# Optimization experiments

Hardware: AMD Instinct MI355X
Metric: run time of the kernel (lower is better)

The kernel has to match this reference:

```python
import jax, jax.numpy as jnp
import numpy as np

TOP_K = 8
RECENCY_DECAY = 0.99
CURRENT_TS = 1.0


def _normalize(x, eps=1e-12):
    # matches torch F.normalize: x / max(||x||_2, eps)
    n = jnp.linalg.norm(x, axis=-1, keepdims=True)
    return x / jnp.maximum(n, eps)


def setup_inputs() -> dict:
    key = jax.random.key(0)
    ks = jax.random.split(key, 7)
    B, N, H = 2048, 65536, 1024
    return {
        "query": jax.random.normal(ks[0], (B, H), dtype=jnp.float32),
        "store": jax.random.normal(ks[1], (N, H), dtype=jnp.float32),
        "importance": jax.random.uniform(ks[2], (N,), dtype=jnp.float32),
        "timestamps": jax.random.uniform(ks[3], (N,), dtype=jnp.float32),
        "Wk": jax.random.normal(ks[4], (H, H), dtype=jnp.float32) / np.sqrt(H),
        "Wv": jax.random.normal(ks[5], (H, H), dtype=jnp.float32) / np.sqrt(H),
        "Wo": jax.random.normal(ks[6], (H, H), dtype=jnp.float32) / np.sqrt(H),
    }


def reference(query, store, importance, timestamps, Wk, Wv, Wo):
    # key/value projections over the full store (Linear, no bias)
    keys = store @ Wk.T          # [N, H]
    vals = store @ Wv.T          # [N, H]

    # recency/importance weighting
    ages = CURRENT_TS - timestamps
    recency = jnp.exp(-jnp.abs(ages) * (1.0 - RECENCY_DECAY))
    weights = recency * (importance + 1.0)
    weights = weights / (weights.sum() + 1e-8)  # [N]

    # cosine similarity scaled by weights
    q_norm = _normalize(query)   # [B, H]
    k_norm = _normalize(keys)    # [N, H]
    sim = (q_norm @ k_norm.T) * weights[None, :]  # [B, N]

    # top-k retrieval + softmax-weighted combine
    topk_sim, topk_idx = jax.lax.top_k(sim, TOP_K)   # [B, k]
    attn = jax.nn.softmax(topk_sim, axis=-1)          # [B, k]
    topk_vals = vals[topk_idx]                        # [B, k, H]
    out = jnp.einsum("bk,bkh->bh", attn, topk_vals)  # [B, H]
    return out @ Wo.T
```

## Files before the change

kernel.cpp:

```cpp
#include <hip/hip_runtime.h>
#include <stdint.h>

typedef _Float16 f16;
typedef _Float16 f16x8 __attribute__((ext_vector_type(8)));
typedef _Float16 f16x4 __attribute__((ext_vector_type(4)));
typedef float    f32x4 __attribute__((ext_vector_type(4)));

#define B_DIM 2048
#define N_DIM 65536
#define H_DIM 1024

typedef const __attribute__((address_space(1))) void g_void;
typedef __attribute__((address_space(3))) void l_void;
__device__ __forceinline__ void glds16(const void* g, void* l) {
    __builtin_amdgcn_global_load_lds((g_void*)g, (l_void*)l, 16, 0, 0);
}

__global__ __launch_bounds__(256) void k_weights(const float* __restrict__ imp,
                                                 const float* __restrict__ ts,
                                                 float* __restrict__ w,
                                                 float* __restrict__ sumw) {
    int i = blockIdx.x * 256 + threadIdx.x;
    float age = 1.0f - ts[i];
    float r = expf(-fabsf(age) * (float)(1.0 - 0.99));
    float wv = r * (imp[i] + 1.0f);
    w[i] = wv;
    for (int off = 32; off; off >>= 1) wv += __shfl_down(wv, off, 64);
    __shared__ float ps[4];
    if ((threadIdx.x & 63) == 0) ps[threadIdx.x >> 6] = wv;
    __syncthreads();
    if (threadIdx.x == 0) atomicAdd(sumw, ps[0] + ps[1] + ps[2] + ps[3]);
}

__global__ __launch_bounds__(256) void k_split(const float* __restrict__ x,
                                               f16* __restrict__ hi, f16* __restrict__ lo) {
    size_t i = (size_t)blockIdx.x * 256 + threadIdx.x;
    float4 v0 = ((const float4*)x)[2 * i];
    float4 v1 = ((const float4*)x)[2 * i + 1];
    float vv[8] = {v0.x, v0.y, v0.z, v0.w, v1.x, v1.y, v1.z, v1.w};
    f16x8 h, l;
#pragma unroll
    for (int j = 0; j < 8; j++) { h[j] = (f16)vv[j]; l[j] = (f16)(vv[j] - (float)h[j]); }
    ((f16x8*)hi)[i] = h;
    ((f16x8*)lo)[i] = l;
}

__global__ __launch_bounds__(256) void k_tohalf(const float* __restrict__ x, f16* __restrict__ h) {
    size_t i = (size_t)blockIdx.x * 256 + threadIdx.x;
    float4 v0 = ((const float4*)x)[2 * i];
    float4 v1 = ((const float4*)x)[2 * i + 1];
    f16x8 o = {(f16)v0.x, (f16)v0.y, (f16)v0.z, (f16)v0.w,
               (f16)v1.x, (f16)v1.y, (f16)v1.z, (f16)v1.w};
    ((f16x8*)h)[i] = o;
}

__global__ __launch_bounds__(256) void k_tsplit(const float* __restrict__ Wm,
                                                f16* __restrict__ th, f16* __restrict__ tl_) {
    __shared__ float tl[64][65];
    const int t = threadIdx.x;
    const int r0 = blockIdx.y * 64, c0 = blockIdx.x * 64;
#pragma unroll
    for (int p = 0; p < 16; ++p) {
        int idx = p * 256 + t;
        int r = idx >> 6, c = idx & 63;
        tl[r][c] = Wm[(size_t)(r0 + r) * H_DIM + c0 + c];
    }
    __syncthreads();
#pragma unroll
    for (int p = 0; p < 16; ++p) {
        int idx = p * 256 + t;
        int oc = idx >> 6, rr = idx & 63;
        float v = tl[rr][oc];
        f16 h = (f16)v;
        th[(size_t)(c0 + oc) * H_DIM + r0 + rr] = h;
        tl_[(size_t)(c0 + oc) * H_DIM + r0 + rr] = (f16)(v - (float)h);
    }
}

__global__ __launch_bounds__(256) void k_qnorm(const float* __restrict__ q,
                                               f16* __restrict__ qh, f16* __restrict__ ql) {
    int b = blockIdx.x, t = threadIdx.x;
    float4 v = ((const float4*)(q + (size_t)b * H_DIM))[t];
    float ss = v.x * v.x + v.y * v.y + v.z * v.z + v.w * v.w;
    for (int off = 32; off; off >>= 1) ss += __shfl_down(ss, off, 64);
    __shared__ float ps[4];
    if ((t & 63) == 0) ps[t >> 6] = ss;
    __syncthreads();
    float tot = ps[0] + ps[1] + ps[2] + ps[3];
    float rn = 1.0f / fmaxf(sqrtf(tot), 1e-12f);
    float o[4] = {v.x * rn, v.y * rn, v.z * rn, v.w * rn};
    f16x4 h, l;
#pragma unroll
    for (int j = 0; j < 4; j++) { h[j] = (f16)o[j]; l[j] = (f16)(o[j] - (float)h[j]); }
    ((f16x4*)(qh + (size_t)b * H_DIM))[t] = h;
    ((f16x4*)(ql + (size_t)b * H_DIM))[t] = l;
}

__global__ __launch_bounds__(256) void k_fin(const float* __restrict__ w,
                                             const float* __restrict__ sumw,
                                             const float* __restrict__ nrm2,
                                             float* __restrict__ sscale) {
    int i = blockIdx.x * 256 + threadIdx.x;
    sscale[i] = w[i] / ((sumw[0] + 1e-8f) * fmaxf(sqrtf(nrm2[i]), 1e-12f));
}


#define RD_A(AB, H)                                                              \
    _Pragma("unroll") for (int mi = 0; mi < 4; ++mi) {                           \
        a[mi][0] = *(const f16x8*)(lds + (AB) + arow + (H)*8192 + mi*2048 + acol0); \
        a[mi][1] = *(const f16x8*)(lds + (AB) + arow + (H)*8192 + mi*2048 + acol1); \
    }

#define RD_B(DST, BB, OFFH)                                                      \
    _Pragma("unroll") for (int nj = 0; nj < 2; ++nj) {                           \
        DST[nj][0] = *(const f16x8*)(lds + (BB) + (OFFH) + brow + nj*2048 + acol0); \
        DST[nj][1] = *(const f16x8*)(lds + (BB) + (OFFH) + brow + nj*2048 + acol1); \
    }

#define PH_PRE()                                                                 \
    __builtin_amdgcn_s_barrier();                                                \
    asm volatile("s_waitcnt lgkmcnt(0)" ::: "memory");                           \
    __builtin_amdgcn_sched_barrier(0);                                           \
    __builtin_amdgcn_s_setprio(1);

#define PH_POST()                                                                \
    __builtin_amdgcn_s_setprio(0);                                               \
    __builtin_amdgcn_s_barrier();

#define MFMA8x2(MH, BV, NB)                                                      \
    _Pragma("unroll") for (int ks = 0; ks < 2; ++ks)                             \
    _Pragma("unroll") for (int mi = 0; mi < 4; ++mi)                             \
    _Pragma("unroll") for (int nj = 0; nj < 2; ++nj)                             \
        acc[(MH)*4 + mi][(NB) + nj] = __builtin_amdgcn_mfma_f32_16x16x32_f16(    \
            a[mi][ks], BV[nj][ks], acc[(MH)*4 + mi][(NB) + nj], 0, 0, 0);

#define TILE_BODY(T, STG, W0STR)                                                 \
  {                                                                              \
    const int cur = (T) & 1;                                                     \
    const int ab = cur * 32768;                                                  \
    const int bb = 65536 + cur * 32768;                                          \
    const int da = (cur ^ 1) * 32768;                                            \
    const int db = 65536 + (cur ^ 1) * 32768;                                    \
    const f16* An = A0; const f16* Bn = Bh; int toffn = 0;                       \
    if (STG) {                                                                   \
        const int tn = (T) + 1;                                                  \
        if constexpr (OUTMODE == 0) {                                            \
            An = (tn < 16) ? A0 : (tn < 32 ? A1 : A0);                           \
            Bn = (tn < 32) ? Bh : Bl;                                            \
            toffn = (tn & 15) * 64;                                              \
        } else { toffn = tn * 64; }                                              \
    }                                                                            \
                                                    \
    RD_A(ab, 0)                                                                  \
    RD_B(b0, bb, 0)                                                              \
    if (STG) {                                                                   \
        glds16(An + aoff0 + toffn, lds + da + tid * 16);                         \
        glds16(An + aoff2 + toffn, lds + da + 16384 + tid * 16);                 \
        glds16(Bn + boffE1 + toffn, lds + db + tid * 16);                        \
        glds16(Bn + boffE2 + toffn, lds + db + 8192 + tid * 16);                 \
    }                                                                            \
    asm volatile("s_waitcnt vmcnt(" W0STR ")" ::: "memory");                     \
    PH_PRE() MFMA8x2(0, b0, 0) PH_POST()                                         \
                                                     \
    RD_B(b1, bb, 16384)                                                          \
    if (STG) {                                                                   \
        glds16(Bn + boffO1 + toffn, lds + db + 16384 + tid * 16);                \
        glds16(Bn + boffO2 + toffn, lds + db + 24576 + tid * 16);                \
        glds16(An + aoff1 + toffn, lds + da + 8192 + tid * 16);                  \
        glds16(An + aoff3 + toffn, lds + da + 24576 + tid * 16);                 \
    }                                                                            \
    PH_PRE() MFMA8x2(0, b1, 2) PH_POST()                                         \
                                                     \
    RD_A(ab, 1)                                                                  \
    PH_PRE() MFMA8x2(1, b1, 2) PH_POST()                                         \
                                                    \
    asm volatile("s_waitcnt vmcnt(4)" ::: "memory");                             \
    PH_PRE() MFMA8x2(1, b0, 0) PH_POST()                                         \
  }

template <int OUTMODE>
__global__ __launch_bounds__(512) void k_gemm8(
    const f16* __restrict__ A0, const f16* __restrict__ A1,
    const f16* __restrict__ Bh, const f16* __restrict__ Bl,
    unsigned int* __restrict__ cand, const float* __restrict__ colscale,
    float* __restrict__ nrm2) {
    __shared__ char lds[131072];
    const int tid = threadIdx.x;

    constexpr int NT = (OUTMODE == 0) ? 48 : 16;

    int m0, n0;
    {
        const int f = blockIdx.x;
        if constexpr (OUTMODE == 0) {
            const int lg = (f & 7) * 128 + (f >> 3);
            m0 = (lg >> 2) * 256; n0 = (lg & 3) * 256;
        } else {
            const int lg = (f & 7) * 256 + (f >> 3);
            m0 = (lg & 7) * 256; n0 = (lg >> 3) * 256;
        }
    }

    const int sr = tid >> 3, ss = tid & 7;
    const int ssw = (ss ^ (sr & 7)) * 8;
    const size_t aoff0 = (size_t)(m0 + sr) * H_DIM + ssw;
    const size_t aoff1 = (size_t)(m0 + 64 + sr) * H_DIM + ssw;
    const size_t aoff2 = (size_t)(m0 + 128 + sr) * H_DIM + ssw;
    const size_t aoff3 = (size_t)(m0 + 192 + sr) * H_DIM + ssw;
    const int nE = (sr >> 5) * 64 + (sr & 31);
    const size_t boffE1 = (size_t)(n0 + nE) * H_DIM + ssw;
    const size_t boffE2 = (size_t)(n0 + nE + 128) * H_DIM + ssw;
    const size_t boffO1 = (size_t)(n0 + nE + 32) * H_DIM + ssw;
    const size_t boffO2 = (size_t)(n0 + nE + 160) * H_DIM + ssw;

    const int lane = tid & 63, wave = tid >> 6;
    const int wr = wave >> 2, wc = wave & 3;
    const int m16 = lane & 15, q4 = lane >> 4;
    const int axor = (lane & 7) << 4;
    const int acol0 = (q4 * 16) ^ axor;
    const int acol1 = (64 + q4 * 16) ^ axor;
    const int arow = (wr * 128 + m16) * 128;
    const int brow = (wc * 32 + m16) * 128;

    f32x4 acc[8][4];
#pragma unroll
    for (int i = 0; i < 8; i++)
#pragma unroll
        for (int j = 0; j < 4; j++) acc[i][j] = (f32x4){0.f, 0.f, 0.f, 0.f};
    f16x8 a[4][2], b0[2][2], b1[2][2];

    glds16(A0 + aoff0, lds + tid * 16);
    glds16(A0 + aoff2, lds + 16384 + tid * 16);
    glds16(Bh + boffE1, lds + 65536 + tid * 16);
    glds16(Bh + boffE2, lds + 65536 + 8192 + tid * 16);
    glds16(Bh + boffO1, lds + 65536 + 16384 + tid * 16);
    glds16(Bh + boffO2, lds + 65536 + 24576 + tid * 16);
    glds16(A0 + aoff1, lds + 8192 + tid * 16);
    glds16(A0 + aoff3, lds + 24576 + tid * 16);
    asm volatile("s_waitcnt vmcnt(4)" ::: "memory");
    __builtin_amdgcn_s_barrier();

    for (int t = 0; t < NT - 1; ++t) TILE_BODY(t, 1, "4")
    TILE_BODY(NT - 1, 0, "0")

    if constexpr (OUTMODE == 0) {
#pragma unroll
        for (int mi = 0; mi < 8; ++mi)
#pragma unroll
            for (int rr = 0; rr < 4; ++rr) {
                float s = 0.f;
#pragma unroll
                for (int njj = 0; njj < 4; ++njj) {
                    float v = acc[mi][njj][rr];
                    s += v * v;
                }
                s += __shfl_xor(s, 1, 64);
                s += __shfl_xor(s, 2, 64);
                s += __shfl_xor(s, 4, 64);
                s += __shfl_xor(s, 8, 64);
                if (m16 == 0)
                    atomicAdd(&nrm2[m0 + wr * 128 + mi * 16 + q4 * 4 + rr], s);
            }
    } else {
        float cs0 = colscale[n0 + wc * 64 + m16];
        float cs1 = colscale[n0 + wc * 64 + 16 + m16];
        float cs2 = colscale[n0 + wc * 64 + 32 + m16];
        float cs3 = colscale[n0 + wc * 64 + 48 + m16];
#pragma unroll
        for (int mi = 0; mi < 8; ++mi)
#pragma unroll
            for (int njj = 0; njj < 4; ++njj) {
                const float c = (njj == 0) ? cs0 : (njj == 1) ? cs1 : (njj == 2) ? cs2 : cs3;
#pragma unroll
                for (int rr = 0; rr < 4; ++rr) acc[mi][njj][rr] *= c;
            }

        float* ldsf = (float*)lds;
        const int r = tid >> 2;
        const int seg = tid & 3;
        const int g5 = tid & 31;
        const int chunkbase = (n0 >> 8) * 8;

#pragma unroll 1
        for (int half = 0; half < 2; ++half) {
            __syncthreads();
            if (wr == half) {
#pragma unroll
                for (int mi = 0; mi < 8; ++mi)
#pragma unroll
                    for (int njj = 0; njj < 4; ++njj)
#pragma unroll
                        for (int rr = 0; rr < 4; ++rr) {
                            int row = mi * 16 + q4 * 4 + rr;
                            int col = wc * 64 + (njj >> 1) * 32 + (njj & 1) * 16 + m16;
                            ldsf[row * 256 + col] = acc[mi][njj][rr];
                        }
            }
            __syncthreads();

            unsigned int tk[8];
#pragma unroll
            for (int i = 0; i < 8; ++i) tk[i] = 0u;
            unsigned int mn = 0u; int mslot = 0;
            for (int jj = 0; jj < 64; ++jj) {
                const int pos = seg * 64 + (jj ^ g5);
                float v = ldsf[r * 256 + pos];
                unsigned int u = __builtin_bit_cast(unsigned int, v);
                u = (u & 0x80000000u) ? ~u : (u | 0x80000000u);
                unsigned int key = (u & 0xFFFFFF00u) | (unsigned)pos;
                if (key > mn) {
#pragma unroll
                    for (int i = 0; i < 8; ++i) tk[i] = (i == mslot) ? key : tk[i];
                    mn = tk[0]; mslot = 0;
#pragma unroll
                    for (int i = 1; i < 8; ++i) { if (tk[i] < mn) { mn = tk[i]; mslot = i; } }
                }
            }
            unsigned int win0, win1, win2, win3, win4, win5, win6, win7;
#pragma unroll
            for (int e = 0; e < 8; ++e) {
                unsigned int lm = tk[0];
#pragma unroll
                for (int i = 1; i < 8; ++i) lm = max(lm, tk[i]);
                unsigned int o1 = max(lm, __shfl_xor(lm, 1, 64));
                unsigned int o2 = max(o1, __shfl_xor(o1, 2, 64));
                if (e == 0) win0 = o2; else if (e == 1) win1 = o2; else if (e == 2) win2 = o2;
                else if (e == 3) win3 = o2; else if (e == 4) win4 = o2; else if (e == 5) win5 = o2;
                else if (e == 6) win6 = o2; else win7 = o2;
#pragma unroll
                for (int i = 0; i < 8; ++i) tk[i] = (tk[i] == o2) ? 0u : tk[i];
            }
            if (seg == 0) {
                const int b = m0 + half * 128 + r;
                uint4* dst = (uint4*)(cand + (size_t)b * 2048 + chunkbase);
                dst[0] = (uint4){win0, win1, win2, win3};
                dst[1] = (uint4){win4, win5, win6, win7};
            }
        }
    }
    (void)A1; (void)Bl; (void)nrm2; (void)colscale; (void)cand;
}

template <int OUTMODE>
__global__ __launch_bounds__(256) void k_gemm64(const f16* __restrict__ A, const f16* __restrict__ Al,
                                                const f16* __restrict__ B, const f16* __restrict__ Bl,
                                                float* __restrict__ of32, f16* __restrict__ of16) {
    __shared__ f16 As[64 * 32];
    __shared__ f16 Bs[128 * 32];
    __shared__ f16 AsL[(OUTMODE == 4) ? 64 * 32 : 1];
    __shared__ f16 BsL[(OUTMODE == 4) ? 128 * 32 : 1];
    const int tid = threadIdx.x;
    const int m0 = blockIdx.y * 64, n0 = blockIdx.x * 128;
    const int r = tid >> 2, c8 = (tid & 3) * 8;
    const f16* ga = A + (size_t)(m0 + r) * H_DIM + c8;
    const f16* gb0 = B + (size_t)(n0 + r) * H_DIM + c8;
    const f16* gb1 = B + (size_t)(n0 + r + 64) * H_DIM + c8;
    const f16 *gal = nullptr, *gbl0 = nullptr, *gbl1 = nullptr;
    if constexpr (OUTMODE == 4) {
        gal = Al + (size_t)(m0 + r) * H_DIM + c8;
        gbl0 = Bl + (size_t)(n0 + r) * H_DIM + c8;
        gbl1 = Bl + (size_t)(n0 + r + 64) * H_DIM + c8;
    }

    const int lane = tid & 63, wave = tid >> 6;
    const int wn = wave * 32;
    const int q4 = lane >> 4, m16 = lane & 15;
    const int aoff = m16 * 32 + q4 * 8;
    const int boff = (wn + m16) * 32 + q4 * 8;

    f32x4 acc[4][2];
#pragma unroll
    for (int i = 0; i < 4; i++)
#pragma unroll
        for (int j = 0; j < 2; j++) acc[i][j] = (f32x4){0.f, 0.f, 0.f, 0.f};

    for (int k0 = 0; k0 < H_DIM; k0 += 32) {
        __syncthreads();
        glds16(ga + k0, As + tid * 8);
        glds16(gb0 + k0, Bs + tid * 8);
        glds16(gb1 + k0, Bs + 2048 + tid * 8);
        if constexpr (OUTMODE == 4) {
            glds16(gal + k0, AsL + tid * 8);
            glds16(gbl0 + k0, BsL + tid * 8);
            glds16(gbl1 + k0, BsL + 2048 + tid * 8);
        }
        __syncthreads();
        f16x8 a[4], b[2], al[4], bl[2];
#pragma unroll
        for (int i = 0; i < 4; i++) a[i] = *(const f16x8*)(As + aoff + i * 512);
#pragma unroll
        for (int j = 0; j < 2; j++) b[j] = *(const f16x8*)(Bs + boff + j * 512);
        if constexpr (OUTMODE == 4) {
#pragma unroll
            for (int i = 0; i < 4; i++) al[i] = *(const f16x8*)(AsL + aoff + i * 512);
#pragma unroll
            for (int j = 0; j < 2; j++) bl[j] = *(const f16x8*)(BsL + boff + j * 512);
        }
#pragma unroll
        for (int i = 0; i < 4; i++)
#pragma unroll
            for (int j = 0; j < 2; j++) {
                if constexpr (OUTMODE == 4) {
                    acc[i][j] = __builtin_amdgcn_mfma_f32_16x16x32_f16(al[i], b[j], acc[i][j], 0, 0, 0);
                    acc[i][j] = __builtin_amdgcn_mfma_f32_16x16x32_f16(a[i], bl[j], acc[i][j], 0, 0, 0);
                }
                acc[i][j] = __builtin_amdgcn_mfma_f32_16x16x32_f16(a[i], b[j], acc[i][j], 0, 0, 0);
            }
    }

#pragma unroll
    for (int i = 0; i < 4; i++) {
        const int rowb = m0 + i * 16 + q4 * 4;
#pragma unroll
        for (int j = 0; j < 2; j++) {
            const int col = n0 + wn + j * 16 + m16;
#pragma unroll
            for (int rr = 0; rr < 4; rr++) {
                const float v = acc[i][j][rr];
                const size_t o = (size_t)(rowb + rr) * H_DIM + col;
                if constexpr (OUTMODE == 2) of16[o] = (f16)v;
                else if constexpr (OUTMODE == 3) of32[o] = v;
                else { of32[o] = v; of16[o] = (f16)v; }
            }
        }
    }
}

__global__ __launch_bounds__(256) void k_merge2(const unsigned int* __restrict__ cand,
                                                const float* __restrict__ qk32,
                                                const float* __restrict__ sscale,
                                                const float* __restrict__ store,
                                                f16* __restrict__ s16) {
    const int b = blockIdx.x, t = threadIdx.x;
    __shared__ unsigned int cl[2048];
    __shared__ unsigned int wmax[2][4];
    __shared__ int c16[16];
    __shared__ float rs[16];
    __shared__ float a8[8];
    __shared__ int i8[8];

    uint4 e0 = ((const uint4*)(cand + (size_t)b * 2048))[t * 2];
    uint4 e1 = ((const uint4*)(cand + (size_t)b * 2048))[t * 2 + 1];
    ((uint4*)cl)[t * 2] = e0;
    ((uint4*)cl)[t * 2 + 1] = e1;
    unsigned int k_[8] = {e0.x, e0.y, e0.z, e0.w, e1.x, e1.y, e1.z, e1.w};
#pragma unroll
    for (int i = 0; i < 8; ++i) k_[i] = (k_[i] & 0xFFFFF800u) | (unsigned)(t * 8 + i);
    __syncthreads();

    const int w = t >> 6;
    for (int rnd = 0; rnd < 16; ++rnd) {
        unsigned int lm = k_[0];
#pragma unroll
        for (int i = 1; i < 8; ++i) lm = max(lm, k_[i]);
        for (int off = 32; off; off >>= 1) lm = max(lm, __shfl_down(lm, off, 64));
        if ((t & 63) == 0) wmax[rnd & 1][w] = lm;
        __syncthreads();
        unsigned int win = max(max(wmax[rnd & 1][0], wmax[rnd & 1][1]),
                               max(wmax[rnd & 1][2], wmax[rnd & 1][3]));
        int idx = (int)(win & 0x7FFu);
        if (t == 0) c16[rnd] = (idx >> 3) * 256 + (int)(cl[idx] & 0xFFu);
        const bool own = (idx >> 3) == t;
#pragma unroll
        for (int i = 0; i < 8; ++i) k_[i] = (own && i == (idx & 7)) ? 0u : k_[i];
    }
    __syncthreads();

    const int g = t >> 4, l16 = t & 15;
    const int idx = c16[g];
    const float* kr = store + (size_t)idx * H_DIM;
    const float* qr = qk32 + (size_t)b * H_DIM;
    float sum = 0.f;
#pragma unroll 8
    for (int j = 0; j < 64; j++) {
        int k = l16 + j * 16;
        sum += qr[k] * kr[k];
    }
    for (int off = 8; off; off >>= 1) sum += __shfl_down(sum, off, 16);
    if (l16 == 0) rs[g] = sum * sscale[idx];
    __syncthreads();

    if (t == 0) {
        float v[16];
        for (int i = 0; i < 16; i++) v[i] = rs[i];
        float av[8]; int ai[8];
        for (int it = 0; it < 8; ++it) {
            float bm = -1e30f; int mi = 0;
            for (int i = 0; i < 16; i++)
                if (v[i] > bm) { bm = v[i]; mi = i; }
            av[it] = bm; ai[it] = c16[mi]; v[mi] = -1e30f;
        }
        float m = av[0], e[8], ssum = 0.f;
        for (int k = 0; k < 8; k++) { e[k] = expf(av[k] - m); ssum += e[k]; }
        for (int k = 0; k < 8; k++) { a8[k] = e[k] / ssum; i8[k] = ai[k]; }
    }
    __syncthreads();

#pragma unroll
    for (int p = 0; p < 4; p++) {
        const int col = t + p * 256;
        float sum2 = 0.f;
#pragma unroll
        for (int k = 0; k < 8; k++) sum2 += a8[k] * store[(size_t)i8[k] * H_DIM + col];
        s16[(size_t)b * H_DIM + col] = (f16)sum2;
    }
}

#define MB (1024ull * 1024ull)
#define OFF_STOREHI (0ull)
#define OFF_STORELO (128ull * MB)
#define OFF_CAND    (256ull * MB)
#define OFF_WKHI    (512ull * MB)
#define OFF_WKLO    (514ull * MB)
#define OFF_WKTH    (516ull * MB)
#define OFF_WKTL    (518ull * MB)
#define OFF_QNHI    (520ull * MB)
#define OFF_QNLO    (524ull * MB)
#define OFF_QK32    (528ull * MB)
#define OFF_QK16    (536ull * MB)
#define OFF_WV16    (540ull * MB)
#define OFF_WO16    (542ull * MB)
#define OFF_W       (544ull * MB)
#define OFF_SSCALE  (544ull * MB + 256ull * 1024ull)
#define OFF_SUMW    (544ull * MB + 512ull * 1024ull)
#define OFF_NRM2    (544ull * MB + 768ull * 1024ull)
#define OFF_S16     (546ull * MB)
#define OFF_T16     (550ull * MB)

extern "C" void kernel_launch(void* const* d_in, const int* in_sizes, int n_in,
                              void* d_out, int out_size, void* d_ws, size_t ws_size,
                              hipStream_t stream) {
    const float* q     = (const float*)d_in[0];
    const float* store = (const float*)d_in[1];
    const float* imp   = (const float*)d_in[2];
    const float* ts    = (const float*)d_in[3];
    const float* Wk    = (const float*)d_in[4];
    const float* Wv    = (const float*)d_in[5];
    const float* Wo    = (const float*)d_in[6];
    float* out = (float*)d_out;
    char* ws = (char*)d_ws;

    f16* storeHi = (f16*)(ws + OFF_STOREHI);
    f16* storeLo = (f16*)(ws + OFF_STORELO);
    unsigned int* cand = (unsigned int*)(ws + OFF_CAND);
    f16* wkHi = (f16*)(ws + OFF_WKHI);
    f16* wkLo = (f16*)(ws + OFF_WKLO);
    f16* wkTh = (f16*)(ws + OFF_WKTH);
    f16* wkTl = (f16*)(ws + OFF_WKTL);
    f16* qnHi = (f16*)(ws + OFF_QNHI);
    f16* qnLo = (f16*)(ws + OFF_QNLO);
    float* qk32 = (float*)(ws + OFF_QK32);
    f16* qk16 = (f16*)(ws + OFF_QK16);
    f16* wv16 = (f16*)(ws + OFF_WV16);
    f16* wo16 = (f16*)(ws + OFF_WO16);
    float* wbuf = (float*)(ws + OFF_W);
    float* sscale = (float*)(ws + OFF_SSCALE);
    float* sumw = (float*)(ws + OFF_SUMW);
    float* nrm2 = (float*)(ws + OFF_NRM2);
    f16* s16 = (f16*)(ws + OFF_S16);
    f16* t16 = (f16*)(ws + OFF_T16);

    hipMemsetAsync(sumw, 0, 4, stream);
    hipMemsetAsync(nrm2, 0, N_DIM * 4, stream);

    k_weights<<<N_DIM / 256, 256, 0, stream>>>(imp, ts, wbuf, sumw);
    k_split<<<(N_DIM * H_DIM) / 2048, 256, 0, stream>>>(store, storeHi, storeLo);
    k_split<<<(H_DIM * H_DIM) / 2048, 256, 0, stream>>>(Wk, wkHi, wkLo);
    k_tsplit<<<dim3(16, 16), 256, 0, stream>>>(Wk, wkTh, wkTl);
    k_tohalf<<<(H_DIM * H_DIM) / 2048, 256, 0, stream>>>(Wv, wv16);
    k_tohalf<<<(H_DIM * H_DIM) / 2048, 256, 0, stream>>>(Wo, wo16);
    k_qnorm<<<B_DIM, 256, 0, stream>>>(q, qnHi, qnLo);

    k_gemm64<4><<<dim3(H_DIM / 128, B_DIM / 64), 256, 0, stream>>>(
        qnHi, qnLo, wkTh, wkTl, qk32, qk16);

    k_gemm8<0><<<1024, 512, 0, stream>>>(storeHi, storeLo, wkHi, wkLo, nullptr, nullptr, nrm2);

    k_fin<<<N_DIM / 256, 256, 0, stream>>>(wbuf, sumw, nrm2, sscale);

    k_gemm8<1><<<2048, 512, 0, stream>>>(qk16, nullptr, storeHi, nullptr, cand, sscale, nullptr);

    k_merge2<<<B_DIM, 256, 0, stream>>>(cand, qk32, sscale, store, s16);

    k_gemm64<2><<<dim3(H_DIM / 128, B_DIM / 64), 256, 0, stream>>>(s16, nullptr, wv16, nullptr, nullptr, t16);
    k_gemm64<3><<<dim3(H_DIM / 128, B_DIM / 64), 256, 0, stream>>>(t16, nullptr, wo16, nullptr, out, nullptr);

    (void)in_sizes; (void)n_in; (void)out_size; (void)ws_size;
}
```

Before: 1.345 ms.

## Replace LDS-staged per-row top-8 with in-register shuffle top-4 per 64-column slice

The GEMM epilogue no longer writes the scaled similarity tile to LDS and runs a serial 64-element insertion top-8 per thread. Each lane now builds a sorted 4-key network from its accumulators and merges top-4 lists across 16 lanes with xor shuffles, writing 4 candidates per 64-column slice. This doubles the candidate buffer (4096 per row) and the merge kernel is adapted to scan 16 keys per thread. The aim is to cut the epilogue's LDS traffic, barriers and serial compare loop. The trade-off is more global candidate traffic and key truncation to 26 bits plus a 6-bit column index, and a 64-column slice holding more than 4 of a row's true top-8 would drop candidates.

```diff
diff --git a/kernel.cpp b/kernel.cpp
--- a/kernel.cpp
+++ b/kernel.cpp
@@ -14,6 +14,12 @@
 typedef __attribute__((address_space(3))) void l_void;
 __device__ __forceinline__ void glds16(const void* g, void* l) {
     __builtin_amdgcn_global_load_lds((g_void*)g, (l_void*)l, 16, 0, 0);
+}
+
+__device__ __forceinline__ unsigned int mkey(float v, unsigned int c6) {
+    unsigned int u = __builtin_bit_cast(unsigned int, v);
+    u ^= (unsigned int)((int)u >> 31) | 0x80000000u;
+    return (u & 0xFFFFFFC0u) | c6;
 }
 
 __global__ __launch_bounds__(256) void k_weights(const float* __restrict__ imp,
@@ -178,6 +184,8 @@
     PH_PRE() MFMA8x2(1, b0, 0) PH_POST()                                         \
   }
 
+#define CMPSWAP(x, y) { unsigned int hi_ = max(x, y), lo_ = min(x, y); x = hi_; y = lo_; }
+
 template <int OUTMODE>
 __global__ __launch_bounds__(512) void k_gemm8(
     const f16* __restrict__ A0, const f16* __restrict__ A1,
@@ -266,77 +274,43 @@
         float cs1 = colscale[n0 + wc * 64 + 16 + m16];
         float cs2 = colscale[n0 + wc * 64 + 32 + m16];
         float cs3 = colscale[n0 + wc * 64 + 48 + m16];
+        const unsigned int c6_0 = (unsigned)m16;
+        const unsigned int c6_1 = (unsigned)(16 + m16);
+        const unsigned int c6_2 = (unsigned)(32 + m16);
+        const unsigned int c6_3 = (unsigned)(48 + m16);
+        const int slice = (n0 >> 6) + wc;
+
 #pragma unroll
         for (int mi = 0; mi < 8; ++mi)
 #pragma unroll
-            for (int njj = 0; njj < 4; ++njj) {
-                const float c = (njj == 0) ? cs0 : (njj == 1) ? cs1 : (njj == 2) ? cs2 : cs3;
-#pragma unroll
-                for (int rr = 0; rr < 4; ++rr) acc[mi][njj][rr] *= c;
-            }
-
-        float* ldsf = (float*)lds;
-        const int r = tid >> 2;
-        const int seg = tid & 3;
-        const int g5 = tid & 31;
-        const int chunkbase = (n0 >> 8) * 8;
-
-#pragma unroll 1
-        for (int half = 0; half < 2; ++half) {
-            __syncthreads();
-            if (wr == half) {
-#pragma unroll
-                for (int mi = 0; mi < 8; ++mi)
-#pragma unroll
-                    for (int njj = 0; njj < 4; ++njj)
-#pragma unroll
-                        for (int rr = 0; rr < 4; ++rr) {
-                            int row = mi * 16 + q4 * 4 + rr;
-                            int col = wc * 64 + (njj >> 1) * 32 + (njj & 1) * 16 + m16;
-                            ldsf[row * 256 + col] = acc[mi][njj][rr];
-                        }
-            }
-            __syncthreads();
-
-            unsigned int tk[8];
-#pragma unroll
-            for (int i = 0; i < 8; ++i) tk[i] = 0u;
-            unsigned int mn = 0u; int mslot = 0;
-            for (int jj = 0; jj < 64; ++jj) {
-                const int pos = seg * 64 + (jj ^ g5);
-                float v = ldsf[r * 256 + pos];
-                unsigned int u = __builtin_bit_cast(unsigned int, v);
-                u = (u & 0x80000000u) ? ~u : (u | 0x80000000u);
-                unsigned int key = (u & 0xFFFFFF00u) | (unsigned)pos;
-                if (key > mn) {
-#pragma unroll
-                    for (int i = 0; i < 8; ++i) tk[i] = (i == mslot) ? key : tk[i];
-                    mn = tk[0]; mslot = 0;
-#pragma unroll
-                    for (int i = 1; i < 8; ++i) { if (tk[i] < mn) { mn = tk[i]; mslot = i; } }
+            for (int rr = 0; rr < 4; ++rr) {
+                unsigned int k0 = mkey(acc[mi][0][rr] * cs0, c6_0);
+                unsigned int k1 = mkey(acc[mi][1][rr] * cs1, c6_1);
+                unsigned int k2 = mkey(acc[mi][2][rr] * cs2, c6_2);
+                unsigned int k3 = mkey(acc[mi][3][rr] * cs3, c6_3);
+                CMPSWAP(k0, k1) CMPSWAP(k2, k3) CMPSWAP(k0, k2) CMPSWAP(k1, k3) CMPSWAP(k1, k2)
+#pragma unroll
+                for (int mm = 1; mm <= 8; mm <<= 1) {
+                    unsigned int p0 = __shfl_xor(k0, mm, 64);
+                    unsigned int p1 = __shfl_xor(k1, mm, 64);
+                    unsigned int p2 = __shfl_xor(k2, mm, 64);
+                    unsigned int p3 = __shfl_xor(k3, mm, 64);
+                    unsigned int L0 = max(k0, p0), H0 = min(k0, p0);
+                    unsigned int L1 = max(k1, p1), H1 = min(k1, p1);
+                    unsigned int L2 = max(k2, p2);
+                    unsigned int L3 = max(k3, p3);
+                    unsigned int r1 = max(H0, L1);
+                    unsigned int m_ = min(H0, L1);
+                    unsigned int r2 = max(m_, max(H1, L2));
+                    unsigned int md = max(min(m_, H1), min(max(m_, H1), L2));
+                    unsigned int r3 = max(md, L3);
+                    k0 = L0; k1 = r1; k2 = r2; k3 = r3;
+                }
+                if (m16 == 0) {
+                    const int b = m0 + wr * 128 + mi * 16 + q4 * 4 + rr;
+                    *(uint4*)(cand + (size_t)b * 4096 + slice * 4) = (uint4){k0, k1, k2, k3};
                 }
             }
-            unsigned int win0, win1, win2, win3, win4, win5, win6, win7;
-#pragma unroll
-            for (int e = 0; e < 8; ++e) {
-                unsigned int lm = tk[0];
-#pragma unroll
-                for (int i = 1; i < 8; ++i) lm = max(lm, tk[i]);
-                unsigned int o1 = max(lm, __shfl_xor(lm, 1, 64));
-                unsigned int o2 = max(o1, __shfl_xor(o1, 2, 64));
-                if (e == 0) win0 = o2; else if (e == 1) win1 = o2; else if (e == 2) win2 = o2;
-                else if (e == 3) win3 = o2; else if (e == 4) win4 = o2; else if (e == 5) win5 = o2;
-                else if (e == 6) win6 = o2; else win7 = o2;
-#pragma unroll
-                for (int i = 0; i < 8; ++i) tk[i] = (tk[i] == o2) ? 0u : tk[i];
-            }
-            if (seg == 0) {
-                const int b = m0 + half * 128 + r;
-                uint4* dst = (uint4*)(cand + (size_t)b * 2048 + chunkbase);
-                dst[0] = (uint4){win0, win1, win2, win3};
-                dst[1] = (uint4){win4, win5, win6, win7};
-            }
-        }
     }
     (void)A1; (void)Bl; (void)nrm2; (void)colscale; (void)cand;
 }
@@ -432,37 +406,43 @@
                                                 const float* __restrict__ store,
                                                 f16* __restrict__ s16) {
     const int b = blockIdx.x, t = threadIdx.x;
-    __shared__ unsigned int cl[2048];
+    __shared__ unsigned int cl[4096];
     __shared__ unsigned int wmax[2][4];
     __shared__ int c16[16];
     __shared__ float rs[16];
     __shared__ float a8[8];
     __shared__ int i8[8];
 
-    uint4 e0 = ((const uint4*)(cand + (size_t)b * 2048))[t * 2];
-    uint4 e1 = ((const uint4*)(cand + (size_t)b * 2048))[t * 2 + 1];
-    ((uint4*)cl)[t * 2] = e0;
-    ((uint4*)cl)[t * 2 + 1] = e1;
-    unsigned int k_[8] = {e0.x, e0.y, e0.z, e0.w, e1.x, e1.y, e1.z, e1.w};
-#pragma unroll
-    for (int i = 0; i < 8; ++i) k_[i] = (k_[i] & 0xFFFFF800u) | (unsigned)(t * 8 + i);
+    const uint4* src = (const uint4*)(cand + (size_t)b * 4096);
+    uint4 e0 = src[t * 4];
+    uint4 e1 = src[t * 4 + 1];
+    uint4 e2 = src[t * 4 + 2];
+    uint4 e3 = src[t * 4 + 3];
+    ((uint4*)cl)[t * 4] = e0;
+    ((uint4*)cl)[t * 4 + 1] = e1;
+    ((uint4*)cl)[t * 4 + 2] = e2;
+    ((uint4*)cl)[t * 4 + 3] = e3;
+    unsigned int k_[16] = {e0.x, e0.y, e0.z, e0.w, e1.x, e1.y, e1.z, e1.w,
+                           e2.x, e2.y, e2.z, e2.w, e3.x, e3.y, e3.z, e3.w};
+#pragma unroll
+    for (int i = 0; i < 16; ++i) k_[i] = (k_[i] & 0xFFFFF000u) | (unsigned)(t * 16 + i);
     __syncthreads();
 
     const int w = t >> 6;
     for (int rnd = 0; rnd < 16; ++rnd) {
         unsigned int lm = k_[0];
 #pragma unroll
-        for (int i = 1; i < 8; ++i) lm = max(lm, k_[i]);
+        for (int i = 1; i < 16; ++i) lm = max(lm, k_[i]);
         for (int off = 32; off; off >>= 1) lm = max(lm, __shfl_down(lm, off, 64));
         if ((t & 63) == 0) wmax[rnd & 1][w] = lm;
         __syncthreads();
         unsigned int win = max(max(wmax[rnd & 1][0], wmax[rnd & 1][1]),
                                max(wmax[rnd & 1][2], wmax[rnd & 1][3]));
-        int idx = (int)(win & 0x7FFu);
-        if (t == 0) c16[rnd] = (idx >> 3) * 256 + (int)(cl[idx] & 0xFFu);
-        const bool own = (idx >> 3) == t;
-#pragma unroll
-        for (int i = 0; i < 8; ++i) k_[i] = (own && i == (idx & 7)) ? 0u : k_[i];
+        int slot = (int)(win & 0xFFFu);
+        if (t == 0) c16[rnd] = (slot >> 2) * 64 + (int)(cl[slot] & 63u);
+        const bool own = (slot >> 4) == t;
+#pragma unroll
+        for (int i = 0; i < 16; ++i) k_[i] = (own && i == (slot & 15)) ? 0u : k_[i];
     }
     __syncthreads();
 
```

Measured after the change: 1.234 ms. 8.2% less time.
